# Kernel tuning notes

Measured on AMD Instinct MI355X. Metric: run time of the kernel, lower is better.

## Reference

```python
import jax, jax.numpy as jnp
import numpy as np

DIM = 1024
NUM_HEADS = 32
HEAD_DIM = 32
T = 2048
SCALE = 0.12
ROT_BASE = HEAD_DIM * 4  # Rotary(head_dim, max_seq_len, head_dim*4)
RMS_EPS = 1.1920929e-07  # torch float32 finfo eps (F.rms_norm default)


def _rms_norm(x):
    ms = jnp.mean(jnp.square(x), axis=-1, keepdims=True)
    return x * jax.lax.rsqrt(ms + RMS_EPS)


def _rotary_tables(seq_len):
    # modded-nanogpt half-truncated rotary: frequencies on first quarter, zeros on second
    quarter = HEAD_DIM // 4
    af = (1.0 / ROT_BASE) ** jnp.linspace(0.0, 1.0, quarter, dtype=jnp.float32)
    af = jnp.concatenate([af, jnp.zeros(quarter, dtype=jnp.float32)])  # [hd/2]
    theta = jnp.arange(seq_len, dtype=jnp.float32)[:, None] * af[None, :]  # [T, hd/2]
    return jnp.cos(theta), jnp.sin(theta)


def _apply_rotary(x, cos, sin):
    # x: [B, T, H, hd]; cos/sin: [T, hd/2]
    x1, x2 = jnp.split(x, 2, axis=-1)
    c = cos[None, :, None, :]
    s = sin[None, :, None, :]
    y1 = x1 * c + x2 * s
    y2 = -x1 * s + x2 * c
    return jnp.concatenate([y1, y2], axis=-1)


def setup_inputs() -> dict:
    key = jax.random.key(0)
    k1, k2, k3, k4 = jax.random.split(key, 4)
    std = 0.5 * DIM ** (-0.5)
    bound = (3.0 ** 0.5) * std
    x = jax.random.normal(k1, (1, T, DIM), dtype=jnp.float32)
    ve = jax.random.normal(k2, (1, T, NUM_HEADS * HEAD_DIM), dtype=jnp.float32)
    qkv_w = jax.random.uniform(k3, (3, NUM_HEADS * HEAD_DIM, DIM), dtype=jnp.float32,
                               minval=-bound, maxval=bound)
    lambdas = jnp.array([0.5, 0.5], dtype=jnp.float32)
    # original zero-inits c_proj; use small random so output/grads are nontrivial
    c_proj_w = jax.random.normal(k4, (DIM, NUM_HEADS * HEAD_DIM), dtype=jnp.float32) * 0.02
    return {"x": x, "ve": ve, "qkv_w": qkv_w, "lambdas": lambdas, "c_proj_w": c_proj_w}


def reference(x, ve, qkv_w, lambdas, c_proj_w):
    B, T_, D = x.shape
    H, hd = NUM_HEADS, HEAD_DIM
    # fused QKV projection: F.linear(x, qkv_w.flatten(end_dim=1))
    w = qkv_w.reshape(3 * H * hd, D)
    qkv = jnp.einsum('btd,ed->bte', x, w).reshape(B, T_, 3 * H, hd)
    q, k, v = jnp.split(qkv, 3, axis=2)  # each [B, T, H, hd]
    q = _rms_norm(q)
    k = _rms_norm(k)
    cos, sin = _rotary_tables(T_)
    q = _apply_rotary(q, cos, sin)
    k = _apply_rotary(k, cos, sin)
    v = lambdas[0] * v + lambdas[1] * ve.reshape(B, T_, H, hd)
    # causal attention with fixed scale 0.12
    scores = jnp.einsum('bqhd,bkhd->bhqk', q, k) * SCALE
    causal = jnp.tril(jnp.ones((T_, T_), dtype=bool))
    scores = jnp.where(causal[None, None, :, :], scores, -jnp.inf)
    attn = jax.nn.softmax(scores, axis=-1)
    y = jnp.einsum('bhqk,bkhd->bqhd', attn, v).reshape(B, T_, H * hd)
    return jnp.einsum('bte,de->btd', y, c_proj_w)
```

## Files before the change

kernel.cpp:

```cpp
#include <hip/hip_runtime.h>
#include <hip/hip_bf16.h>

#define NHEADS 32
#define HD_ 32
#define TSEQ 2048
#define SCALE_ 0.12f
#define LOG2E_ 1.44269504088896f
#define RMS_EPS_ 1.1920929e-07f

typedef unsigned short ushort_t;
typedef __bf16 bf16_t;
typedef __attribute__((ext_vector_type(8))) bf16_t bf16x8;
typedef __attribute__((ext_vector_type(4))) float f32x4;
typedef __attribute__((ext_vector_type(8))) unsigned short u16x8;

__device__ __forceinline__ ushort_t f2bfn(float f){
    __hip_bfloat16 b = __float2bfloat16(f);
    return *reinterpret_cast<ushort_t*>(&b);
}
__device__ __forceinline__ float bf2f(ushort_t s){
    union { unsigned u; float f; } v; v.u = ((unsigned)s) << 16;
    return v.f;
}
__device__ __forceinline__ float fexp2(float x){
#if __has_builtin(__builtin_amdgcn_exp2f)
    return __builtin_amdgcn_exp2f(x);
#else
    return exp2f(x);
#endif
}
__device__ __forceinline__ void gld16(const void* g, void* l){
    __builtin_amdgcn_global_load_lds(
        (const __attribute__((address_space(1))) unsigned int*)g,
        (__attribute__((address_space(3))) unsigned int*)l,
        16, 0, 0);
}

__global__ __launch_bounds__(256) void k_prep(const float* __restrict__ x,
                                              const float* __restrict__ qkw,
                                              const float* __restrict__ cpw,
                                              ushort_t* __restrict__ xb,
                                              ushort_t* __restrict__ wb,
                                              ushort_t* __restrict__ cpb,
                                              float* __restrict__ cost,
                                              float* __restrict__ sint)
{
    const int n1 = TSEQ * 1024 / 4, n2 = 3 * 1024 * 1024 / 4, n3 = 1024 * 1024 / 4;
    int i = blockIdx.x * 256 + threadIdx.x;
    if (i < n1 + n2 + n3){
        const float* src; ushort_t* dst; int j = i;
        if (j < n1){ src = x; dst = xb; }
        else if (j < n1 + n2){ j -= n1; src = qkw; dst = wb; }
        else { j -= n1 + n2; src = cpw; dst = cpb; }
        float4 v = ((const float4*)src)[j];
        ushort4 o;
        o.x = f2bfn(v.x); o.y = f2bfn(v.y); o.z = f2bfn(v.z); o.w = f2bfn(v.w);
        ((ushort4*)dst)[j] = o;
    } else {
        int g = i - (n1 + n2 + n3);
        if (g < TSEQ * 16){
            int t = g >> 4, ii = g & 15;
            float c = 1.0f, s = 0.0f;
            if (ii < 8){
                float af = powf(1.0f / 128.0f, (float)ii * (1.0f / 7.0f));
                sincosf((float)t * af, &s, &c);
            }
            cost[g] = c; sint[g] = s;
        }
    }
}

template<int BM, int BN, bool OUT_BF16>
__global__ __launch_bounds__(256) void k_gemm64(const ushort_t* __restrict__ A,
                                                const ushort_t* __restrict__ B,
                                                void* __restrict__ C,
                                                int M, int N, int K)
{
    constexpr int MI = BM / 32, NI = BN / 32;
    __shared__ __align__(16) ushort_t As[2][BM * 64];
    __shared__ __align__(16) ushort_t Bs[2][BN * 64];
    const int tid = threadIdx.x;
    const int lane = tid & 63;
    const int w = tid >> 6;
    const int wr = w >> 1, wc = w & 1;
    const int l15 = lane & 15, hi = lane >> 4;
    const int m0 = blockIdx.y * BM, n0 = blockIdx.x * BN;
    const int srow = lane >> 3, scol = (lane & 7) * 8;

    f32x4 acc[MI][NI] = {};

    auto stage = [&](int k0, int buf){
        #pragma unroll
        for (int i = 0; i < BM / 32; ++i){
            int c = w * (BM / 32) + i;
            gld16(&A[(size_t)(m0 + c * 8 + srow) * K + k0 + scol], &As[buf][c * 512]);
        }
        #pragma unroll
        for (int i = 0; i < BN / 32; ++i){
            int c = w * (BN / 32) + i;
            gld16(&B[(size_t)(n0 + c * 8 + srow) * K + k0 + scol], &Bs[buf][c * 512]);
        }
    };

    stage(0, 0);
    int cur = 0;
    for (int k0 = 0; k0 < K; k0 += 64){
        __syncthreads();
        if (k0 + 64 < K) stage(k0 + 64, cur ^ 1);
        bf16x8 af[MI][2], bfr[NI][2];
        #pragma unroll
        for (int mi = 0; mi < MI; ++mi)
            #pragma unroll
            for (int sub = 0; sub < 2; ++sub)
                af[mi][sub] = *(const bf16x8*)&As[cur][(wr * (BM/2) + mi * 16 + l15) * 64 + sub * 32 + hi * 8];
        #pragma unroll
        for (int ni = 0; ni < NI; ++ni)
            #pragma unroll
            for (int sub = 0; sub < 2; ++sub)
                bfr[ni][sub] = *(const bf16x8*)&Bs[cur][(wc * (BN/2) + ni * 16 + l15) * 64 + sub * 32 + hi * 8];
        #pragma unroll
        for (int sub = 0; sub < 2; ++sub)
            #pragma unroll
            for (int mi = 0; mi < MI; ++mi)
                #pragma unroll
                for (int ni = 0; ni < NI; ++ni)
                    acc[mi][ni] = __builtin_amdgcn_mfma_f32_16x16x32_bf16(af[mi][sub], bfr[ni][sub], acc[mi][ni], 0, 0, 0);
        cur ^= 1;
    }

    #pragma unroll
    for (int mi = 0; mi < MI; ++mi)
        #pragma unroll
        for (int ni = 0; ni < NI; ++ni)
            #pragma unroll
            for (int r = 0; r < 4; ++r){
                int row = m0 + wr * (BM/2) + mi * 16 + hi * 4 + r;
                int col = n0 + wc * (BN/2) + ni * 16 + l15;
                float v = acc[mi][ni][r];
                if (OUT_BF16) ((ushort_t*)C)[(size_t)row * N + col] = f2bfn(v);
                else          ((float*)C)[(size_t)row * N + col] = v;
            }
}

__global__ __launch_bounds__(256) void k_fuse(const ushort_t* __restrict__ qkvb,
                                              const float* __restrict__ ve,
                                              const float* __restrict__ lam,
                                              const float* __restrict__ cost,
                                              const float* __restrict__ sint,
                                              ushort_t* __restrict__ qb,
                                              ushort_t* __restrict__ kb,
                                              ushort_t* __restrict__ vtb)
{
    const int h  = blockIdx.y;
    const int t0 = blockIdx.x * 64;
    const int tid = threadIdx.x;
    const int tl = tid >> 2;
    const int dg = tid & 3;
    const int t  = t0 + tl;

    __shared__ __align__(16) float vtile[32 * 65];

    float cs[8], sn[8];
    #pragma unroll
    for (int j = 0; j < 8; ++j){
        int ci = (dg * 8 + j) & 15;
        cs[j] = cost[t * 16 + ci];
        sn[j] = sint[t * 16 + ci];
    }
    const float sgn = (dg < 2) ? 1.0f : -1.0f;

    #pragma unroll
    for (int which = 0; which < 2; ++which){
        u16x8 raw = *(const u16x8*)&qkvb[(size_t)t * 3072 + which * 1024 + h * 32 + dg * 8];
        float v[8];
        float ss = 0.0f;
        #pragma unroll
        for (int j = 0; j < 8; ++j){ v[j] = bf2f(raw[j]); ss += v[j] * v[j]; }
        ss += __shfl_xor(ss, 1);
        ss += __shfl_xor(ss, 2);
        const float inv = rsqrtf(ss * (1.0f / 32.0f) + RMS_EPS_);
        const float scl = (which == 0) ? SCALE_ * LOG2E_ : 1.0f;
        u16x8 o;
        #pragma unroll
        for (int j = 0; j < 8; ++j){
            float nv = v[j] * inv;
            float p  = __shfl_xor(nv, 2);
            o[j] = f2bfn((nv * cs[j] + sgn * p * sn[j]) * scl);
        }
        ushort_t* dst = (which == 0) ? qb : kb;
        *(u16x8*)&dst[((size_t)h * TSEQ + t) * 32 + dg * 8] = o;
    }

    const float l0 = lam[0], l1 = lam[1];
    {
        u16x8 raw = *(const u16x8*)&qkvb[(size_t)t * 3072 + 2048 + h * 32 + dg * 8];
        const float4* vep = (const float4*)&ve[(size_t)t * 1024 + h * 32 + dg * 8];
        float4 a = vep[0], b = vep[1];
        float vef[8] = {a.x, a.y, a.z, a.w, b.x, b.y, b.z, b.w};
        #pragma unroll
        for (int j = 0; j < 8; ++j)
            vtile[(dg * 8 + j) * 65 + tl] = l0 * bf2f(raw[j]) + l1 * vef[j];
    }
    __syncthreads();
    {
        const int d = tid >> 3, jj = tid & 7;
        u16x8 o;
        #pragma unroll
        for (int e = 0; e < 8; ++e)
            o[e] = f2bfn(vtile[d * 65 + jj * 8 + e]);
        *(u16x8*)&vtb[((size_t)h * HD_ + d) * TSEQ + t0 + jj * 8] = o;
    }
}

template<bool MASK>
__device__ __forceinline__ void chain_step(const bf16x8* kf, const bf16x8* vv0, const bf16x8* vv1,
                                           ushort_t* pb, const bf16x8& qf,
                                           int kb0, int qrow, int l15, int hi,
                                           f32x4& a0, f32x4& a1, float& lp)
{
    f32x4 s[4];
    #pragma unroll
    for (int ni = 0; ni < 4; ++ni){
        f32x4 z = {0.f, 0.f, 0.f, 0.f};
        s[ni] = __builtin_amdgcn_mfma_f32_16x16x32_bf16(kf[ni], qf, z, 0, 0, 0);
    }
    if (MASK){
        const int relc = qrow - kb0 - 4 * hi;
        #pragma unroll
        for (int ni = 0; ni < 4; ++ni)
            #pragma unroll
            for (int r = 0; r < 4; ++r)
                if (16 * ni + r > relc) s[ni][r] = -1e30f;
    }
    float ps = 0.f;
    #pragma unroll
    for (int ni = 0; ni < 4; ++ni)
        #pragma unroll
        for (int r = 0; r < 4; ++r){
            float p = fexp2(s[ni][r]);
            s[ni][r] = p;
            ps += p;
        }
    lp += ps;
    #pragma unroll
    for (int ni = 0; ni < 4; ++ni){
        ushort4 pk;
        pk.x = f2bfn(s[ni][0]); pk.y = f2bfn(s[ni][1]);
        pk.z = f2bfn(s[ni][2]); pk.w = f2bfn(s[ni][3]);
        *(ushort4*)&pb[l15 * 72 + ni * 16 + hi * 4] = pk;
    }
    #pragma unroll
    for (int kk = 0; kk < 2; ++kk){
        bf16x8 pf = *(const bf16x8*)&pb[l15 * 72 + kk * 32 + hi * 8];
        a0 = __builtin_amdgcn_mfma_f32_16x16x32_bf16(vv0[kk], pf, a0, 0, 0, 0);
        a1 = __builtin_amdgcn_mfma_f32_16x16x32_bf16(vv1[kk], pf, a1, 0, 0, 0);
    }
}

__global__ __launch_bounds__(256) void k_attn(const ushort_t* __restrict__ qb,
                                              const ushort_t* __restrict__ kb,
                                              const ushort_t* __restrict__ vtb,
                                              ushort_t* __restrict__ yb)
{
    const int bid = blockIdx.x;
    const int xcd = bid & 7, idx = bid >> 3;
    const int h = xcd * 4 + (idx >> 4);
    const int b = idx & 15;
    const int tid = threadIdx.x;
    const int w = tid >> 6, lane = tid & 63;
    const int l15 = lane & 15, hi = lane >> 4;

    __shared__ __align__(16) ushort_t Kbuf[2][64 * 32];
    __shared__ __align__(16) ushort_t Vbuf[2][32 * 64];
    __shared__ __align__(16) ushort_t Pbuf[4][2][16 * 72];

    const ushort_t* kb_h = kb + (size_t)h * TSEQ * HD_;
    const ushort_t* vt_h = vtb + (size_t)h * HD_ * TSEQ;
    const ushort_t* qb_h = qb + (size_t)h * TSEQ * HD_;

    const int qtA = b, qtB = 31 - b;
    const int qwA = qtA * 64 + w * 16, qwB = qtB * 64 + w * 16;
    const bf16x8 qfA = *(const bf16x8*)&qb_h[(size_t)(qwA + l15) * 32 + hi * 8];
    const bf16x8 qfB = *(const bf16x8*)&qb_h[(size_t)(qwB + l15) * 32 + hi * 8];

    const int krow_in = w * 16 + (lane >> 2);
    const int kslot_in = (lane & 3) ^ ((krow_in >> 1) & 3);
    const int vrow_in = w * 8 + (lane >> 3);
    const int vslot_in = (lane & 7) ^ (vrow_in & 7);

    auto stage = [&](int kt, int buf){
        int kb0 = kt * 64;
        gld16(&kb_h[(size_t)(kb0 + krow_in) * 32 + kslot_in * 8], &Kbuf[buf][w * 512]);
        gld16(&vt_h[(size_t)vrow_in * TSEQ + kb0 + vslot_in * 8], &Vbuf[buf][w * 512]);
    };

    const int kswz = hi ^ ((l15 >> 1) & 3);
    const int vswz = l15 & 7;

    f32x4 a0A = {0.f,0.f,0.f,0.f}, a1A = a0A, a0B = a0A, a1B = a0A;
    float lpA = 0.f, lpB = 0.f;
    ushort_t* pbB = &Pbuf[w][0][0];
    ushort_t* pbA = &Pbuf[w][1][0];

    stage(0, 0);
    int cur = 0;
    const int nB = qtB + 1;
    for (int kt = 0; kt < nB; ++kt){
        __syncthreads();
        if (kt + 1 < nB) stage(kt + 1, cur ^ 1);
        const int kb0 = kt * 64;
        bf16x8 kf[4], vv0[2], vv1[2];
        #pragma unroll
        for (int ni = 0; ni < 4; ++ni)
            kf[ni] = *(const bf16x8*)&Kbuf[cur][(16 * ni + l15) * 32 + kswz * 8];
        #pragma unroll
        for (int kk = 0; kk < 2; ++kk){
            vv0[kk] = *(const bf16x8*)&Vbuf[cur][l15 * 64 + ((kk * 4 + hi) ^ vswz) * 8];
            vv1[kk] = *(const bf16x8*)&Vbuf[cur][(16 + l15) * 64 + ((kk * 4 + hi) ^ vswz) * 8];
        }
        if (kt < qtB)
            chain_step<false>(kf, vv0, vv1, pbB, qfB, kb0, qwB + l15, l15, hi, a0B, a1B, lpB);
        else
            chain_step<true >(kf, vv0, vv1, pbB, qfB, kb0, qwB + l15, l15, hi, a0B, a1B, lpB);
        if (kt < qtA)
            chain_step<false>(kf, vv0, vv1, pbA, qfA, kb0, qwA + l15, l15, hi, a0A, a1A, lpA);
        else if (kt == qtA)
            chain_step<true >(kf, vv0, vv1, pbA, qfA, kb0, qwA + l15, l15, hi, a0A, a1A, lpA);
        cur ^= 1;
    }

    #pragma unroll
    for (int which = 0; which < 2; ++which){
        f32x4 a0 = which ? a0B : a0A;
        f32x4 a1 = which ? a1B : a1A;
        float lp = which ? lpB : lpA;
        int qw = which ? qwB : qwA;
        lp += __shfl_xor(lp, 16);
        lp += __shfl_xor(lp, 32);
        float inv = 1.0f / lp;
        ushort4 o0, o1;
        o0.x = f2bfn(a0[0]*inv); o0.y = f2bfn(a0[1]*inv);
        o0.z = f2bfn(a0[2]*inv); o0.w = f2bfn(a0[3]*inv);
        o1.x = f2bfn(a1[0]*inv); o1.y = f2bfn(a1[1]*inv);
        o1.z = f2bfn(a1[2]*inv); o1.w = f2bfn(a1[3]*inv);
        size_t base = (size_t)(qw + l15) * 1024 + h * 32;
        *(ushort4*)&yb[base + hi * 4]      = o0;
        *(ushort4*)&yb[base + 16 + hi * 4] = o1;
    }
}

extern "C" void kernel_launch(void* const* d_in, const int* in_sizes, int n_in,
                              void* d_out, int out_size, void* d_ws, size_t ws_size,
                              hipStream_t stream)
{
    const float* x   = (const float*)d_in[0];
    const float* ve  = (const float*)d_in[1];
    const float* qkw = (const float*)d_in[2];
    const float* lam = (const float*)d_in[3];
    const float* cpw = (const float*)d_in[4];

    char* ws = (char*)d_ws;
    size_t o = 0;
    auto take = [&](size_t bytes) -> char* {
        char* p = ws + o; o += (bytes + 255) & ~(size_t)255; return p;
    };
    ushort_t* xb   = (ushort_t*)take((size_t)TSEQ * 1024 * 2);
    ushort_t* wb   = (ushort_t*)take((size_t)3072 * 1024 * 2);
    ushort_t* cpb  = (ushort_t*)take((size_t)1024 * 1024 * 2);
    ushort_t* qkvb = (ushort_t*)take((size_t)TSEQ * 3072 * 2);
    float*    cost = (float*)take((size_t)TSEQ * 16 * 4);
    float*    sint = (float*)take((size_t)TSEQ * 16 * 4);
    ushort_t* qb   = (ushort_t*)take((size_t)NHEADS * TSEQ * HD_ * 2);
    ushort_t* kb   = (ushort_t*)take((size_t)NHEADS * TSEQ * HD_ * 2);
    ushort_t* vtb  = (ushort_t*)take((size_t)NHEADS * HD_ * TSEQ * 2);
    ushort_t* yb   = xb;

    const int prep_items = (TSEQ * 1024 + 3 * 1024 * 1024 + 1024 * 1024) / 4 + TSEQ * 16;
    k_prep<<<(prep_items + 255) / 256, 256, 0, stream>>>(x, qkw, cpw, xb, wb, cpb, cost, sint);
    k_gemm64<64, 128, true ><<<dim3(3072 / 128, TSEQ / 64), 256, 0, stream>>>(xb, wb, qkvb, TSEQ, 3072, 1024);
    k_fuse<<<dim3(TSEQ / 64, NHEADS), 256, 0, stream>>>(qkvb, ve, lam, cost, sint, qb, kb, vtb);
    k_attn<<<512, 256, 0, stream>>>(qb, kb, vtb, yb);
    k_gemm64<64, 64, false><<<dim3(1024 / 64, TSEQ / 64), 256, 0, stream>>>(yb, cpb, (float*)d_out, TSEQ, 1024, 1024);
}
```

Baseline: 161.5 us.

## Use 128x128 QKV GEMM tiles, 128-key attention stages, and MFMA priority hints

The QKV projection GEMM moves from 64x128 tiles with K-step 64 to 128x128 tiles with K-step 32 and launch bounds allowing 3 blocks per CU. The aim is more reuse per loaded tile and fewer blocks. The attention kernel now stages 128 keys per barrier instead of 64, halving the number of syncs. It shares one P buffer per wave across both query chains and drops the K swizzle. setprio hints are wrapped around the MFMA sections. Risks include LDS bank conflicts on the unswizzled K reads, a possible race on the shared P buffer between the two chains, and loads past the final key block, which the extra 8 KB of workspace padding covers.

New measurement: 159.3 us. About the same (-1.3%).

```diff
diff --git a/kernel.cpp b/kernel.cpp
--- a/kernel.cpp
+++ b/kernel.cpp
@@ -70,34 +70,86 @@
     }
 }
 
-template<int BM, int BN, bool OUT_BF16>
-__global__ __launch_bounds__(256) void k_gemm64(const ushort_t* __restrict__ A,
-                                                const ushort_t* __restrict__ B,
-                                                void* __restrict__ C,
-                                                int M, int N, int K)
-{
-    constexpr int MI = BM / 32, NI = BN / 32;
-    __shared__ __align__(16) ushort_t As[2][BM * 64];
-    __shared__ __align__(16) ushort_t Bs[2][BN * 64];
+__global__ __launch_bounds__(256, 3) void k_gemm128(const ushort_t* __restrict__ A,
+                                                    const ushort_t* __restrict__ B,
+                                                    ushort_t* __restrict__ C,
+                                                    int M, int N, int K)
+{
+    __shared__ __align__(16) ushort_t As[2][128 * 32];
+    __shared__ __align__(16) ushort_t Bs[2][128 * 32];
     const int tid = threadIdx.x;
     const int lane = tid & 63;
     const int w = tid >> 6;
     const int wr = w >> 1, wc = w & 1;
     const int l15 = lane & 15, hi = lane >> 4;
-    const int m0 = blockIdx.y * BM, n0 = blockIdx.x * BN;
+    const int m0 = blockIdx.y * 128, n0 = blockIdx.x * 128;
+    const int srow = lane >> 2, scol = (lane & 3) * 8;
+
+    f32x4 acc[4][4] = {};
+
+    auto stage = [&](int k0, int buf){
+        #pragma unroll
+        for (int i = 0; i < 2; ++i){
+            int c = w * 2 + i;
+            gld16(&A[(size_t)(m0 + c * 16 + srow) * K + k0 + scol], &As[buf][c * 512]);
+            gld16(&B[(size_t)(n0 + c * 16 + srow) * K + k0 + scol], &Bs[buf][c * 512]);
+        }
+    };
+
+    stage(0, 0);
+    int cur = 0;
+    for (int k0 = 0; k0 < K; k0 += 32){
+        __syncthreads();
+        if (k0 + 32 < K) stage(k0 + 32, cur ^ 1);
+        bf16x8 af[4], bfr[4];
+        #pragma unroll
+        for (int mi = 0; mi < 4; ++mi)
+            af[mi] = *(const bf16x8*)&As[cur][(wr * 64 + mi * 16 + l15) * 32 + hi * 8];
+        #pragma unroll
+        for (int ni = 0; ni < 4; ++ni)
+            bfr[ni] = *(const bf16x8*)&Bs[cur][(wc * 64 + ni * 16 + l15) * 32 + hi * 8];
+        #pragma unroll
+        for (int mi = 0; mi < 4; ++mi)
+            #pragma unroll
+            for (int ni = 0; ni < 4; ++ni)
+                acc[mi][ni] = __builtin_amdgcn_mfma_f32_16x16x32_bf16(af[mi], bfr[ni], acc[mi][ni], 0, 0, 0);
+        cur ^= 1;
+    }
+
+    #pragma unroll
+    for (int mi = 0; mi < 4; ++mi)
+        #pragma unroll
+        for (int ni = 0; ni < 4; ++ni)
+            #pragma unroll
+            for (int r = 0; r < 4; ++r){
+                int row = m0 + wr * 64 + mi * 16 + hi * 4 + r;
+                int col = n0 + wc * 64 + ni * 16 + l15;
+                C[(size_t)row * N + col] = f2bfn(acc[mi][ni][r]);
+            }
+}
+
+__global__ __launch_bounds__(256) void k_gemm_out(const ushort_t* __restrict__ A,
+                                                  const ushort_t* __restrict__ B,
+                                                  float* __restrict__ C,
+                                                  int M, int N, int K)
+{
+    __shared__ __align__(16) ushort_t As[2][64 * 64];
+    __shared__ __align__(16) ushort_t Bs[2][64 * 64];
+    const int tid = threadIdx.x;
+    const int lane = tid & 63;
+    const int w = tid >> 6;
+    const int wr = w >> 1, wc = w & 1;
+    const int l15 = lane & 15, hi = lane >> 4;
+    const int m0 = blockIdx.y * 64, n0 = blockIdx.x * 64;
     const int srow = lane >> 3, scol = (lane & 7) * 8;
 
-    f32x4 acc[MI][NI] = {};
+    f32x4 acc[2][2] = {};
 
     auto stage = [&](int k0, int buf){
         #pragma unroll
-        for (int i = 0; i < BM / 32; ++i){
-            int c = w * (BM / 32) + i;
+        for (int i = 0; i < 2; ++i){
+            int c = w * 2 + i;
             gld16(&A[(size_t)(m0 + c * 8 + srow) * K + k0 + scol], &As[buf][c * 512]);
-        }
-        #pragma unroll
-        for (int i = 0; i < BN / 32; ++i){
-            int c = w * (BN / 32) + i;
             gld16(&B[(size_t)(n0 + c * 8 + srow) * K + k0 + scol], &Bs[buf][c * 512]);
         }
     };
@@ -107,38 +159,36 @@
     for (int k0 = 0; k0 < K; k0 += 64){
         __syncthreads();
         if (k0 + 64 < K) stage(k0 + 64, cur ^ 1);
-        bf16x8 af[MI][2], bfr[NI][2];
-        #pragma unroll
-        for (int mi = 0; mi < MI; ++mi)
+        bf16x8 af[2][2], bfr[2][2];
+        #pragma unroll
+        for (int mi = 0; mi < 2; ++mi)
             #pragma unroll
             for (int sub = 0; sub < 2; ++sub)
-                af[mi][sub] = *(const bf16x8*)&As[cur][(wr * (BM/2) + mi * 16 + l15) * 64 + sub * 32 + hi * 8];
-        #pragma unroll
-        for (int ni = 0; ni < NI; ++ni)
+                af[mi][sub] = *(const bf16x8*)&As[cur][(wr * 32 + mi * 16 + l15) * 64 + sub * 32 + hi * 8];
+        #pragma unroll
+        for (int ni = 0; ni < 2; ++ni)
             #pragma unroll
             for (int sub = 0; sub < 2; ++sub)
-                bfr[ni][sub] = *(const bf16x8*)&Bs[cur][(wc * (BN/2) + ni * 16 + l15) * 64 + sub * 32 + hi * 8];
+                bfr[ni][sub] = *(const bf16x8*)&Bs[cur][(wc * 32 + ni * 16 + l15) * 64 + sub * 32 + hi * 8];
         #pragma unroll
         for (int sub = 0; sub < 2; ++sub)
             #pragma unroll
-            for (int mi = 0; mi < MI; ++mi)
+            for (int mi = 0; mi < 2; ++mi)
                 #pragma unroll
-                for (int ni = 0; ni < NI; ++ni)
+                for (int ni = 0; ni < 2; ++ni)
                     acc[mi][ni] = __builtin_amdgcn_mfma_f32_16x16x32_bf16(af[mi][sub], bfr[ni][sub], acc[mi][ni], 0, 0, 0);
         cur ^= 1;
     }
 
     #pragma unroll
-    for (int mi = 0; mi < MI; ++mi)
-        #pragma unroll
-        for (int ni = 0; ni < NI; ++ni)
+    for (int mi = 0; mi < 2; ++mi)
+        #pragma unroll
+        for (int ni = 0; ni < 2; ++ni)
             #pragma unroll
             for (int r = 0; r < 4; ++r){
-                int row = m0 + wr * (BM/2) + mi * 16 + hi * 4 + r;
-                int col = n0 + wc * (BN/2) + ni * 16 + l15;
-                float v = acc[mi][ni][r];
-                if (OUT_BF16) ((ushort_t*)C)[(size_t)row * N + col] = f2bfn(v);
-                else          ((float*)C)[(size_t)row * N + col] = v;
+                int row = m0 + wr * 32 + mi * 16 + hi * 4 + r;
+                int col = n0 + wc * 32 + ni * 16 + l15;
+                C[(size_t)row * N + col] = acc[mi][ni][r];
             }
 }
 
@@ -219,11 +269,13 @@
                                            f32x4& a0, f32x4& a1, float& lp)
 {
     f32x4 s[4];
+    __builtin_amdgcn_s_setprio(1);
     #pragma unroll
     for (int ni = 0; ni < 4; ++ni){
         f32x4 z = {0.f, 0.f, 0.f, 0.f};
         s[ni] = __builtin_amdgcn_mfma_f32_16x16x32_bf16(kf[ni], qf, z, 0, 0, 0);
     }
+    __builtin_amdgcn_s_setprio(0);
     if (MASK){
         const int relc = qrow - kb0 - 4 * hi;
         #pragma unroll
@@ -249,12 +301,14 @@
         pk.z = f2bfn(s[ni][2]); pk.w = f2bfn(s[ni][3]);
         *(ushort4*)&pb[l15 * 72 + ni * 16 + hi * 4] = pk;
     }
+    __builtin_amdgcn_s_setprio(1);
     #pragma unroll
     for (int kk = 0; kk < 2; ++kk){
         bf16x8 pf = *(const bf16x8*)&pb[l15 * 72 + kk * 32 + hi * 8];
         a0 = __builtin_amdgcn_mfma_f32_16x16x32_bf16(vv0[kk], pf, a0, 0, 0, 0);
         a1 = __builtin_amdgcn_mfma_f32_16x16x32_bf16(vv1[kk], pf, a1, 0, 0, 0);
     }
+    __builtin_amdgcn_s_setprio(0);
 }
 
 __global__ __launch_bounds__(256) void k_attn(const ushort_t* __restrict__ qb,
@@ -270,9 +324,9 @@
     const int w = tid >> 6, lane = tid & 63;
     const int l15 = lane & 15, hi = lane >> 4;
 
-    __shared__ __align__(16) ushort_t Kbuf[2][64 * 32];
-    __shared__ __align__(16) ushort_t Vbuf[2][32 * 64];
-    __shared__ __align__(16) ushort_t Pbuf[4][2][16 * 72];
+    __shared__ __align__(16) ushort_t Kbuf[2][128 * 32];
+    __shared__ __align__(16) ushort_t Vbuf[2][32 * 128];
+    __shared__ __align__(16) ushort_t Pbuf[4][16 * 72];
 
     const ushort_t* kb_h = kb + (size_t)h * TSEQ * HD_;
     const ushort_t* vt_h = vtb + (size_t)h * HD_ * TSEQ;
@@ -283,49 +337,56 @@
     const bf16x8 qfA = *(const bf16x8*)&qb_h[(size_t)(qwA + l15) * 32 + hi * 8];
     const bf16x8 qfB = *(const bf16x8*)&qb_h[(size_t)(qwB + l15) * 32 + hi * 8];
 
-    const int krow_in = w * 16 + (lane >> 2);
-    const int kslot_in = (lane & 3) ^ ((krow_in >> 1) & 3);
-    const int vrow_in = w * 8 + (lane >> 3);
-    const int vslot_in = (lane & 7) ^ (vrow_in & 7);
-
-    auto stage = [&](int kt, int buf){
-        int kb0 = kt * 64;
-        gld16(&kb_h[(size_t)(kb0 + krow_in) * 32 + kslot_in * 8], &Kbuf[buf][w * 512]);
-        gld16(&vt_h[(size_t)vrow_in * TSEQ + kb0 + vslot_in * 8], &Vbuf[buf][w * 512]);
+    const int kck0 = w * 2;
+    auto stage = [&](int bs, int buf){
+        const int kb0 = bs * 128;
+        #pragma unroll
+        for (int i = 0; i < 2; ++i){
+            int c = kck0 + i;
+            int krow = c * 16 + (lane >> 2);
+            gld16(&kb_h[(size_t)(kb0 + krow) * 32 + (lane & 3) * 8], &Kbuf[buf][c * 512]);
+            int vrow = c * 4 + (lane >> 4);
+            int vj = (lane & 15) ^ (vrow & 7);
+            gld16(&vt_h[(size_t)vrow * TSEQ + kb0 + vj * 8], &Vbuf[buf][c * 512]);
+        }
     };
-
-    const int kswz = hi ^ ((l15 >> 1) & 3);
-    const int vswz = l15 & 7;
 
     f32x4 a0A = {0.f,0.f,0.f,0.f}, a1A = a0A, a0B = a0A, a1B = a0A;
     float lpA = 0.f, lpB = 0.f;
-    ushort_t* pbB = &Pbuf[w][0][0];
-    ushort_t* pbA = &Pbuf[w][1][0];
+    ushort_t* pb = &Pbuf[w][0];
+
+    const int nA = qtA + 1, nB = qtB + 1;
+    const int NB2 = (nB + 1) >> 1;
 
     stage(0, 0);
     int cur = 0;
-    const int nB = qtB + 1;
-    for (int kt = 0; kt < nB; ++kt){
+    for (int bs = 0; bs < NB2; ++bs){
         __syncthreads();
-        if (kt + 1 < nB) stage(kt + 1, cur ^ 1);
-        const int kb0 = kt * 64;
-        bf16x8 kf[4], vv0[2], vv1[2];
-        #pragma unroll
-        for (int ni = 0; ni < 4; ++ni)
-            kf[ni] = *(const bf16x8*)&Kbuf[cur][(16 * ni + l15) * 32 + kswz * 8];
-        #pragma unroll
-        for (int kk = 0; kk < 2; ++kk){
-            vv0[kk] = *(const bf16x8*)&Vbuf[cur][l15 * 64 + ((kk * 4 + hi) ^ vswz) * 8];
-            vv1[kk] = *(const bf16x8*)&Vbuf[cur][(16 + l15) * 64 + ((kk * 4 + hi) ^ vswz) * 8];
-        }
-        if (kt < qtB)
-            chain_step<false>(kf, vv0, vv1, pbB, qfB, kb0, qwB + l15, l15, hi, a0B, a1B, lpB);
-        else
-            chain_step<true >(kf, vv0, vv1, pbB, qfB, kb0, qwB + l15, l15, hi, a0B, a1B, lpB);
-        if (kt < qtA)
-            chain_step<false>(kf, vv0, vv1, pbA, qfA, kb0, qwA + l15, l15, hi, a0A, a1A, lpA);
-        else if (kt == qtA)
-            chain_step<true >(kf, vv0, vv1, pbA, qfA, kb0, qwA + l15, l15, hi, a0A, a1A, lpA);
+        if (bs + 1 < NB2) stage(bs + 1, cur ^ 1);
+        #pragma unroll
+        for (int sub = 0; sub < 2; ++sub){
+            const int kt = bs * 2 + sub;
+            if (kt >= nB) break;
+            const int kb0 = kt * 64;
+            bf16x8 kf[4], vv0[2], vv1[2];
+            #pragma unroll
+            for (int ni = 0; ni < 4; ++ni)
+                kf[ni] = *(const bf16x8*)&Kbuf[cur][(sub * 64 + ni * 16 + l15) * 32 + hi * 8];
+            #pragma unroll
+            for (int kk = 0; kk < 2; ++kk){
+                int sl = sub * 8 + kk * 4 + hi;
+                vv0[kk] = *(const bf16x8*)&Vbuf[cur][l15 * 128 + (sl ^ (l15 & 7)) * 8];
+                vv1[kk] = *(const bf16x8*)&Vbuf[cur][(16 + l15) * 128 + (sl ^ (l15 & 7)) * 8];
+            }
+            if (kt < qtB)
+                chain_step<false>(kf, vv0, vv1, pb, qfB, kb0, qwB + l15, l15, hi, a0B, a1B, lpB);
+            else
+                chain_step<true >(kf, vv0, vv1, pb, qfB, kb0, qwB + l15, l15, hi, a0B, a1B, lpB);
+            if (kt < qtA)
+                chain_step<false>(kf, vv0, vv1, pb, qfA, kb0, qwA + l15, l15, hi, a0A, a1A, lpA);
+            else if (kt == qtA)
+                chain_step<true >(kf, vv0, vv1, pb, qfA, kb0, qwA + l15, l15, hi, a0A, a1A, lpA);
+        }
         cur ^= 1;
     }
 
@@ -371,14 +432,14 @@
     float*    cost = (float*)take((size_t)TSEQ * 16 * 4);
     float*    sint = (float*)take((size_t)TSEQ * 16 * 4);
     ushort_t* qb   = (ushort_t*)take((size_t)NHEADS * TSEQ * HD_ * 2);
-    ushort_t* kb   = (ushort_t*)take((size_t)NHEADS * TSEQ * HD_ * 2);
-    ushort_t* vtb  = (ushort_t*)take((size_t)NHEADS * HD_ * TSEQ * 2);
+    ushort_t* kb   = (ushort_t*)take((size_t)NHEADS * TSEQ * HD_ * 2 + 8192);
+    ushort_t* vtb  = (ushort_t*)take((size_t)NHEADS * HD_ * TSEQ * 2 + 8192);
     ushort_t* yb   = xb;
 
     const int prep_items = (TSEQ * 1024 + 3 * 1024 * 1024 + 1024 * 1024) / 4 + TSEQ * 16;
     k_prep<<<(prep_items + 255) / 256, 256, 0, stream>>>(x, qkw, cpw, xb, wb, cpb, cost, sint);
-    k_gemm64<64, 128, true ><<<dim3(3072 / 128, TSEQ / 64), 256, 0, stream>>>(xb, wb, qkvb, TSEQ, 3072, 1024);
+    k_gemm128<<<dim3(3072 / 128, TSEQ / 128), 256, 0, stream>>>(xb, wb, qkvb, TSEQ, 3072, 1024);
     k_fuse<<<dim3(TSEQ / 64, NHEADS), 256, 0, stream>>>(qkvb, ve, lam, cost, sint, qb, kb, vtb);
     k_attn<<<512, 256, 0, stream>>>(qb, kb, vtb, yb);
-    k_gemm64<64, 64, false><<<dim3(1024 / 64, TSEQ / 64), 256, 0, stream>>>(yb, cpb, (float*)d_out, TSEQ, 1024, 1024);
-}
+    k_gemm_out<<<dim3(1024 / 64, TSEQ / 64), 256, 0, stream>>>(yb, cpb, (float*)d_out, TSEQ, 1024, 1024);
+}
```
